# Performance work log

Measured on AMD Instinct MI355X. Metric: run time of the kernel, lower is better.

Reference implementation:

```python
import jax, jax.numpy as jnp
import numpy as np


def setup_inputs() -> dict:
    key = jax.random.key(0)
    ks = jax.random.split(key, 10)
    B, C, T, H, W = 1, 512, 8, 32, 32
    x = jax.random.normal(ks[0], (B, C, T, H, W), dtype=jnp.float32)
    gamma = jnp.ones((C,), dtype=jnp.float32)  # RMSNorm gamma (shape (C,1,1,1) in torch)
    std = 0.02
    wq = jax.random.normal(ks[1], (C, C), dtype=jnp.float32) * std
    bq = jnp.zeros((C,), dtype=jnp.float32)
    wk = jax.random.normal(ks[2], (C, C), dtype=jnp.float32) * std
    bk = jnp.zeros((C,), dtype=jnp.float32)
    wv = jax.random.normal(ks[3], (C, C), dtype=jnp.float32) * std
    bv = jnp.zeros((C,), dtype=jnp.float32)
    wo = jax.random.normal(ks[4], (C, C), dtype=jnp.float32) * std
    bo = jnp.zeros((C,), dtype=jnp.float32)
    return {"x": x, "gamma": gamma, "wq": wq, "bq": bq, "wk": wk, "bk": bk,
            "wv": wv, "bv": bv, "wo": wo, "bo": bo}


def _conv1(w, b, h):
    # 1x1x1 Conv3d == per-position channel matmul. h: [B,C,T,H,W]
    return jnp.einsum('oc,bcthw->bothw', w, h) + b[None, :, None, None, None]


def reference(x, gamma, wq, bq, wk, bk, wv, bv, wo, bo):
    B, C, T, H, W = x.shape
    n_hw = H * W
    S = T * n_hw
    scale = C ** 0.5

    # RMS norm over channel dim (F.normalize dim=1, eps=1e-12) * sqrt(C) * gamma
    norm = jnp.sqrt(jnp.sum(x * x, axis=1, keepdims=True))
    xn = x / jnp.maximum(norm, 1e-12) * scale * gamma[None, :, None, None, None]

    q = _conv1(wq, bq, xn).reshape(B, C, S).transpose(0, 2, 1)  # [B,S,C]
    k = _conv1(wk, bk, xn).reshape(B, C, S).transpose(0, 2, 1)
    v = _conv1(wv, bv, xn).reshape(B, C, S).transpose(0, 2, 1)

    # frame-block causal mask: token i (frame fi) attends to j with frame fj <= fi
    frame = jnp.arange(S) // n_hw
    allowed = frame[None, :] <= frame[:, None]  # [S,S] bool

    scores = jnp.einsum('bic,bjc->bij', q, k) / np.sqrt(C).astype(np.float32)
    scores = jnp.where(allowed[None], scores, -jnp.inf)
    attn = jax.nn.softmax(scores, axis=-1)
    o = jnp.einsum('bij,bjc->bic', attn, v)  # [B,S,C]

    o = o.transpose(0, 2, 1).reshape(B, C, T, H, W)
    out = _conv1(wo, bo, o) + x
    return out
```

## Files before the change

kernel.cpp:

```cpp
#include <hip/hip_runtime.h>
#include <stdint.h>


typedef __bf16 bf16;
typedef __bf16 bf16x8 __attribute__((ext_vector_type(8)));
typedef float f32x4 __attribute__((ext_vector_type(4)));
typedef uint32_t u32;
typedef uint32_t u32x2 __attribute__((ext_vector_type(2)));

#define MFMA16(a, b, c) __builtin_amdgcn_mfma_f32_16x16x32_bf16((a), (b), (c), 0, 0, 0)

__device__ __forceinline__ u32 pack2(float a, float b) {
  union { bf16 h[2]; u32 u; } x;
  x.h[0] = (bf16)a;
  x.h[1] = (bf16)b;
  return x.u;
}

__device__ __forceinline__ void async_copy16(const bf16* gsrc, bf16* ldst) {
  __builtin_amdgcn_global_load_lds(
      (const __attribute__((address_space(1))) void*)gsrc,
      (__attribute__((address_space(3))) void*)ldst, 16, 0, 0);
}

__global__ void cvt_w_kernel(const float* __restrict__ a, const float* __restrict__ b,
                             const float* __restrict__ c, const float* __restrict__ d,
                             bf16* __restrict__ out) {
  int i = blockIdx.x * 256 + threadIdx.x;
  const int N = 512 * 512;
  out[i]         = (bf16)a[i];
  out[N + i]     = (bf16)b[i];
  out[2 * N + i] = (bf16)c[i];
  out[3 * N + i] = (bf16)d[i];
}

__global__ __launch_bounds__(256) void rmsnorm_kernel(const float* __restrict__ x,
                                                      const float* __restrict__ gamma,
                                                      bf16* __restrict__ xn) {
  const int S = 8192;
  __shared__ float sums[4][64];
  int ts = threadIdx.x & 63, tc = threadIdx.x >> 6;
  int s = blockIdx.x * 64 + ts;
  float acc = 0.f;
  for (int c = tc * 128; c < tc * 128 + 128; ++c) {
    float v = x[(size_t)c * S + s];
    acc += v * v;
  }
  sums[tc][ts] = acc;
  __syncthreads();
  float tot = sums[0][ts] + sums[1][ts] + sums[2][ts] + sums[3][ts];
  float kk = 22.62741699796952f / fmaxf(sqrtf(tot), 1e-12f);
  for (int c0 = tc * 128; c0 < tc * 128 + 128; c0 += 8) {
    bf16x8 o;
#pragma unroll
    for (int j = 0; j < 8; ++j) o[j] = (bf16)(x[(size_t)(c0 + j) * S + s] * kk * gamma[c0 + j]);
    *(bf16x8*)(xn + (size_t)s * 512 + c0) = o;
  }
}

template <int EPI>
__global__ __launch_bounds__(256, 2) void gemm_nt_kernel(const bf16* __restrict__ A,
                                                         const bf16* __restrict__ B,
                                                         const float* __restrict__ bias0,
                                                         const float* __restrict__ bias1,
                                                         const float* __restrict__ resid,
                                                         void* __restrict__ Cout0,
                                                         void* __restrict__ Cout1, int M, int N,
                                                         int nbn) {
  __shared__ bf16 a_lds[2][128 * 64];
  __shared__ bf16 b_lds[2][128 * 64];
  const int K = 512;
  int bm = blockIdx.x / nbn, bn = blockIdx.x % nbn;
  int m0 = bm * 128, n0 = bn * 128;
  int tid = threadIdx.x, lane = tid & 63;
  int wid = tid >> 6;
  int wm = (wid >> 1) * 64, wn = (wid & 1) * 64;
  int l15 = lane & 15, l4 = lane >> 4;
  f32x4 acc[4][4];
#pragma unroll
  for (int i = 0; i < 4; ++i)
#pragma unroll
    for (int j = 0; j < 4; ++j) acc[i][j] = (f32x4){0.f, 0.f, 0.f, 0.f};

  auto stage = [&](int buf, int k0) {
#pragma unroll
    for (int j = 0; j < 4; ++j) {
      int r = wid * 32 + j * 8 + (lane >> 3);
      int cs = ((lane & 7) ^ (r & 7)) << 3;
      async_copy16(A + (size_t)(m0 + r) * K + k0 + cs, &a_lds[buf][(wid * 32 + j * 8) << 6]);
      async_copy16(B + (size_t)(n0 + r) * K + k0 + cs, &b_lds[buf][(wid * 32 + j * 8) << 6]);
    }
  };

  stage(0, 0);
  int buf = 0;
  int swk = l15 & 7;
  for (int t = 0; t < 8; ++t) {
    if (t < 7) {
      stage(buf ^ 1, (t + 1) * 64);
      asm volatile("s_waitcnt vmcnt(8)" ::: "memory");
    } else {
      asm volatile("s_waitcnt vmcnt(0)" ::: "memory");
    }
    __builtin_amdgcn_s_barrier();
#pragma unroll
    for (int kk = 0; kk < 2; ++kk) {
      bf16x8 af[4], bfr[4];
#pragma unroll
      for (int i = 0; i < 4; ++i)
        af[i] = *(bf16x8*)(&a_lds[buf][((wm + i * 16 + l15) << 6) + (((kk * 4 + l4) ^ swk) << 3)]);
#pragma unroll
      for (int j = 0; j < 4; ++j)
        bfr[j] = *(bf16x8*)(&b_lds[buf][((wn + j * 16 + l15) << 6) + (((kk * 4 + l4) ^ swk) << 3)]);
#pragma unroll
      for (int i = 0; i < 4; ++i)
#pragma unroll
        for (int j = 0; j < 4; ++j) acc[i][j] = MFMA16(af[i], bfr[j], acc[i][j]);
    }
    __builtin_amdgcn_s_barrier();
    buf ^= 1;
  }
#pragma unroll
  for (int i = 0; i < 4; ++i)
#pragma unroll
    for (int j = 0; j < 4; ++j) {
      int col = n0 + wn + j * 16 + l15;
#pragma unroll
      for (int r = 0; r < 4; ++r) {
        int row = m0 + wm + i * 16 + l4 * 4 + r;
        float v = acc[i][j][r];
        if (EPI == 0) {
          bf16* o = (bf16*)(col < 512 ? Cout0 : Cout1);
          const float* bb = col < 512 ? bias0 : bias1;
          int cc = col & 511;
          o[(size_t)row * 512 + cc] = (bf16)(v + bb[cc]);
        } else if (EPI == 1) {
          size_t idx = (size_t)row * N + col;
          ((float*)Cout0)[idx] = v + bias0[row] + resid[idx];
        } else {
          ((bf16*)Cout0)[(size_t)row * N + col] = (bf16)(v + bias0[row]);
        }
      }
    }
}

__global__ __launch_bounds__(256, 2) void attn_kernel(const bf16* __restrict__ Qg,
                                                      const bf16* __restrict__ Kg,
                                                      const bf16* __restrict__ VT,
                                                      bf16* __restrict__ Oat,
                                                      bf16* __restrict__ Opart,
                                                      float2* __restrict__ mlbuf) {
  const float SC2 = 1.4426950408889634f / 22.627416997969522f;
  __shared__ bf16 k_lds[32 * 512];
  __shared__ bf16 vt_lds[512 * 32];

  int b = (blockIdx.x & 7) * 64 + (blockIdx.x >> 3);
  int f = 0, cxe = 0, np = 1;
  while (b >= 16 * np) { b -= 16 * np; cxe += np - 1; ++f; np = (f < 4) ? f + 1 : f; }
  int p = b >> 4, qi = b & 15;
  int q0 = f * 1024 + qi * 64;
  int ntf = (f + 1) * 32;
  int t0 = (p * ntf) / np, t1 = ((p + 1) * ntf) / np;

  int tid = threadIdx.x, wid = tid >> 6, lane = tid & 63;
  int l15 = lane & 15, l4 = lane >> 4;

  int qrow = q0 + wid * 16 + l15;
  bf16x8 qreg[16];
#pragma unroll
  for (int ks = 0; ks < 16; ++ks)
    qreg[ks] = *(const bf16x8*)(Qg + (size_t)qrow * 512 + ks * 32 + l4 * 8);

  f32x4 oacc[32];
#pragma unroll
  for (int i = 0; i < 32; ++i) oacc[i] = (f32x4){0.f, 0.f, 0.f, 0.f};
  float lsum = 0.f;

  auto stageK = [&](int t) {
    int kv0 = t * 32;
#pragma unroll
    for (int i = 0; i < 8; ++i) {
      int rr = wid * 8 + i;
      int g = (rr & 3) | (((rr >> 3) & 1) << 2);
      async_copy16(Kg + (((size_t)(kv0 + rr)) << 9) + ((lane ^ g) << 3), &k_lds[rr << 9]);
    }
  };
  auto stageV = [&](int t) {
    int kv0 = t * 32;
#pragma unroll
    for (int i = 0; i < 8; ++i) {
      int rr = wid * 8 + i;
      async_copy16(VT + (size_t)(rr * 16 + (lane >> 2)) * 8192 + kv0 +
                       (((lane & 3) ^ ((lane >> 3) & 3)) << 3),
                   &vt_lds[rr << 9]);
    }
  };

  stageK(t0);
  stageV(t0);

  int gk = (l15 & 3) | (((l15 >> 2) & 1) << 2);
  int ra = ((l15 >> 2) * 8 + (l15 & 3)) << 9;
  int rb = ra + (4 << 9);
  int svw = (l15 >> 1) & 3;

  for (int t = t0; t < t1; ++t) {
    asm volatile("s_waitcnt vmcnt(8)" ::: "memory");
    __builtin_amdgcn_s_barrier();

    f32x4 sacca = {0.f, 0.f, 0.f, 0.f}, saccb = sacca;
    __builtin_amdgcn_s_setprio(1);
#pragma unroll
    for (int ks = 0; ks < 16; ++ks) {
      int c0 = ((ks * 4 + l4) ^ gk) << 3;
      bf16x8 a0 = *(const bf16x8*)(k_lds + ra + c0);
      bf16x8 a1 = *(const bf16x8*)(k_lds + rb + c0);
      sacca = MFMA16(a0, qreg[ks], sacca);
      saccb = MFMA16(a1, qreg[ks], saccb);
    }
    __builtin_amdgcn_s_setprio(0);

    float pra[4], prb[4];
    float ps = 0.f;
#pragma unroll
    for (int r = 0; r < 4; ++r) {
      pra[r] = exp2f(sacca[r] * SC2);
      prb[r] = exp2f(saccb[r] * SC2);
      ps += pra[r] + prb[r];
    }
    lsum += ps;

    union { u32 d[4]; bf16x8 v; } pf;
    pf.d[0] = pack2(pra[0], pra[1]);
    pf.d[1] = pack2(pra[2], pra[3]);
    pf.d[2] = pack2(prb[0], prb[1]);
    pf.d[3] = pack2(prb[2], prb[3]);

    asm volatile("s_waitcnt vmcnt(0)" ::: "memory");
    __builtin_amdgcn_s_barrier();

    if (t + 1 < t1) stageK(t + 1);

    __builtin_amdgcn_s_setprio(1);
#pragma unroll
    for (int df = 0; df < 32; ++df) {
      bf16x8 vf = *(const bf16x8*)(vt_lds + (df * 16 + l15) * 32 + ((l4 ^ svw) << 3));
      oacc[df] = MFMA16(vf, pf.v, oacc[df]);
    }
    __builtin_amdgcn_s_setprio(0);

    __builtin_amdgcn_s_barrier();
    if (t + 1 < t1) stageV(t + 1);
  }

  lsum += __shfl_xor(lsum, 16);
  lsum += __shfl_xor(lsum, 32);

  int qr = q0 + wid * 16 + l15;
  bf16* op = (p == 0) ? Oat + (size_t)qr * 512
                      : Opart + ((size_t)(cxe + p - 1) * 1024 + (qr & 1023)) * 512;
#pragma unroll
  for (int df = 0; df < 32; ++df) {
    u32x2 w2 = {pack2(oacc[df][0], oacc[df][1]), pack2(oacc[df][2], oacc[df][3])};
    *(u32x2*)(op + df * 16 + l4 * 4) = w2;
  }
  if (l4 == 0) mlbuf[p * 8192 + qr] = make_float2(0.f, lsum);
}

__global__ void combine_kernel(const bf16* __restrict__ Opart, const float2* __restrict__ ml,
                               bf16* __restrict__ O) {
  int i = blockIdx.x * 256 + threadIdx.x;
  int row = i >> 6, dc = (i & 63) * 8;
  int f = row >> 10;
  int np = f + (f < 4 ? 1 : 0);
  int cxe = f * (f - 1) / 2 - (f > 4 ? f - 4 : 0);
  float2 m0 = ml[row];
  float mm = m0.x;
  for (int p = 1; p < np; ++p) mm = fmaxf(mm, ml[p * 8192 + row].x);
  float acc[8];
  float denom;
  {
    float w = exp2f(m0.x - mm);
    denom = w * m0.y;
    bf16x8 o = *(const bf16x8*)(O + (size_t)row * 512 + dc);
#pragma unroll
    for (int j = 0; j < 8; ++j) acc[j] = w * (float)o[j];
  }
  int rowin = row & 1023;
  for (int p = 1; p < np; ++p) {
    float2 mp = ml[p * 8192 + row];
    float w = exp2f(mp.x - mm);
    denom += w * mp.y;
    bf16x8 o = *(const bf16x8*)(Opart + ((size_t)(cxe + p - 1) * 1024 + rowin) * 512 + dc);
#pragma unroll
    for (int j = 0; j < 8; ++j) acc[j] += w * (float)o[j];
  }
  float inv = 1.f / denom;
  bf16x8 r;
#pragma unroll
  for (int j = 0; j < 8; ++j) r[j] = (bf16)(acc[j] * inv);
  *(bf16x8*)(O + (size_t)row * 512 + dc) = r;
}

extern "C" void kernel_launch(void* const* d_in, const int* in_sizes, int n_in, void* d_out,
                              int out_size, void* d_ws, size_t ws_size, hipStream_t stream) {
  (void)in_sizes; (void)n_in; (void)out_size; (void)ws_size;
  const float* x = (const float*)d_in[0];
  const float* gamma = (const float*)d_in[1];
  const float* wq = (const float*)d_in[2];
  const float* bq = (const float*)d_in[3];
  const float* wk = (const float*)d_in[4];
  const float* bk = (const float*)d_in[5];
  const float* wv = (const float*)d_in[6];
  const float* bv = (const float*)d_in[7];
  const float* wo = (const float*)d_in[8];
  const float* bo = (const float*)d_in[9];

  const size_t SC = (size_t)8192 * 512;
  bf16* wq_b = (bf16*)d_ws;
  bf16* wk_b = wq_b + 262144;
  bf16* wv_b = wk_b + 262144;
  bf16* wo_b = wv_b + 262144;
  bf16* xn_oat = wo_b + 262144;
  bf16* q = xn_oat + SC;
  bf16* k = q + SC;
  bf16* vt = k + SC;
  bf16* opart = vt + SC;
  float2* ml = (float2*)(opart + (size_t)24 * 1024 * 512);

  cvt_w_kernel<<<1024, 256, 0, stream>>>(wq, wk, wv, wo, wq_b);
  rmsnorm_kernel<<<128, 256, 0, stream>>>(x, gamma, xn_oat);
  gemm_nt_kernel<0><<<512, 256, 0, stream>>>(xn_oat, wq_b, bq, bk, nullptr, q, k, 8192, 1024, 8);
  gemm_nt_kernel<2><<<256, 256, 0, stream>>>(wv_b, xn_oat, bv, nullptr, nullptr, vt, nullptr, 512,
                                             8192, 64);
  attn_kernel<<<512, 256, 0, stream>>>(q, k, vt, xn_oat, opart, ml);
  combine_kernel<<<2048, 256, 0, stream>>>(opart, ml, xn_oat);
  gemm_nt_kernel<1><<<256, 256, 0, stream>>>(wo_b, xn_oat, bo, nullptr, x, d_out, nullptr, 512,
                                             8192, 64);
}
```

Baseline: 212.8 us.

## Share P tiles via LDS so each wave computes a D-slice for all query rows

Each wave writes its bf16 probability fragment to LDS, then reads all four waves' fragments and computes the PV product for a 128-wide slice of the head dimension across all 64 query rows. Before, each wave read the full 512-wide V^T tile from LDS for its own 16 rows. Now each V fragment is loaded once and reused across four MFMAs, cutting LDS read traffic for V by about four times. The cost is an extra LDS write and read of P plus an lgkmcnt wait before the barrier. The output store layout is reorganised to match.

Result: slower. 268.9 us (+26.3%).

```diff
diff --git a/kernel.cpp b/kernel.cpp
--- a/kernel.cpp
+++ b/kernel.cpp
@@ -153,6 +153,7 @@
   const float SC2 = 1.4426950408889634f / 22.627416997969522f;
   __shared__ bf16 k_lds[32 * 512];
   __shared__ bf16 vt_lds[512 * 32];
+  __shared__ bf16 p_lds[4][16 * 40];
 
   int b = (blockIdx.x & 7) * 64 + (blockIdx.x >> 3);
   int f = 0, cxe = 0, np = 1;
@@ -235,17 +236,23 @@
     pf.d[1] = pack2(pra[2], pra[3]);
     pf.d[2] = pack2(prb[0], prb[1]);
     pf.d[3] = pack2(prb[2], prb[3]);
-
-    asm volatile("s_waitcnt vmcnt(0)" ::: "memory");
+    *(bf16x8*)(&p_lds[wid][l15 * 40 + l4 * 8]) = pf.v;
+
+    asm volatile("s_waitcnt vmcnt(0) lgkmcnt(0)" ::: "memory");
     __builtin_amdgcn_s_barrier();
 
     if (t + 1 < t1) stageK(t + 1);
 
+    bf16x8 pfr[4];
+#pragma unroll
+    for (int s = 0; s < 4; ++s) pfr[s] = *(const bf16x8*)(&p_lds[s][l15 * 40 + l4 * 8]);
     __builtin_amdgcn_s_setprio(1);
 #pragma unroll
-    for (int df = 0; df < 32; ++df) {
-      bf16x8 vf = *(const bf16x8*)(vt_lds + (df * 16 + l15) * 32 + ((l4 ^ svw) << 3));
-      oacc[df] = MFMA16(vf, pf.v, oacc[df]);
+    for (int dt = 0; dt < 8; ++dt) {
+      bf16x8 vf =
+          *(const bf16x8*)(vt_lds + (wid * 128 + dt * 16 + l15) * 32 + ((l4 ^ svw) << 3));
+#pragma unroll
+      for (int s = 0; s < 4; ++s) oacc[dt * 4 + s] = MFMA16(vf, pfr[s], oacc[dt * 4 + s]);
     }
     __builtin_amdgcn_s_setprio(0);
 
@@ -256,15 +263,19 @@
   lsum += __shfl_xor(lsum, 16);
   lsum += __shfl_xor(lsum, 32);
 
-  int qr = q0 + wid * 16 + l15;
-  bf16* op = (p == 0) ? Oat + (size_t)qr * 512
-                      : Opart + ((size_t)(cxe + p - 1) * 1024 + (qr & 1023)) * 512;
-#pragma unroll
-  for (int df = 0; df < 32; ++df) {
-    u32x2 w2 = {pack2(oacc[df][0], oacc[df][1]), pack2(oacc[df][2], oacc[df][3])};
-    *(u32x2*)(op + df * 16 + l4 * 4) = w2;
-  }
-  if (l4 == 0) mlbuf[p * 8192 + qr] = make_float2(0.f, lsum);
+  bf16* obase = (p == 0) ? Oat : Opart + ((size_t)(cxe + p - 1) * 1024) * 512;
+#pragma unroll
+  for (int s = 0; s < 4; ++s) {
+    int qr = q0 + s * 16 + l15;
+    int qloc = (p == 0) ? qr : (qr & 1023);
+    bf16* op = obase + (size_t)qloc * 512 + wid * 128 + l4 * 4;
+#pragma unroll
+    for (int dt = 0; dt < 8; ++dt) {
+      f32x4 o = oacc[dt * 4 + s];
+      *(u32x2*)(op + dt * 16) = (u32x2){pack2(o[0], o[1]), pack2(o[2], o[3])};
+    }
+  }
+  if (l4 == 0) mlbuf[p * 8192 + q0 + wid * 16 + l15] = make_float2(0.f, lsum);
 }
 
 __global__ void combine_kernel(const bf16* __restrict__ Opart, const float2* __restrict__ ml,
```

## Merge prep and projection launches, defer softmax normalization into output GEMM

Applied to the files above, without the earlier changes.

Weight conversion and RMSNorm now run in one launch, split by block index. The Q/K and V projection GEMMs are likewise merged into a single launch. The combine kernel drops the max-based rescaling, because the stored max is always zero. It now only sums partial outputs for rows that have several partials, and writes a per-row inverse denominator. The output GEMM applies that inverse per token column in its epilogue. This removes two kernel launches and some elementwise work in combine, at the cost of a bf16 intermediate that is no longer normalized and some branching in the merged kernels.

Result: slower. 220.0 us (+3.4%).

```diff
diff --git a/kernel.cpp b/kernel.cpp
--- a/kernel.cpp
+++ b/kernel.cpp
@@ -23,22 +23,25 @@
       (__attribute__((address_space(3))) void*)ldst, 16, 0, 0);
 }
 
-__global__ void cvt_w_kernel(const float* __restrict__ a, const float* __restrict__ b,
-                             const float* __restrict__ c, const float* __restrict__ d,
-                             bf16* __restrict__ out) {
-  int i = blockIdx.x * 256 + threadIdx.x;
-  const int N = 512 * 512;
-  out[i]         = (bf16)a[i];
-  out[N + i]     = (bf16)b[i];
-  out[2 * N + i] = (bf16)c[i];
-  out[3 * N + i] = (bf16)d[i];
-}
-
-__global__ __launch_bounds__(256) void rmsnorm_kernel(const float* __restrict__ x,
-                                                      const float* __restrict__ gamma,
-                                                      bf16* __restrict__ xn) {
+__global__ __launch_bounds__(256) void prep_kernel(const float* __restrict__ x,
+                                                   const float* __restrict__ gamma,
+                                                   bf16* __restrict__ xn,
+                                                   const float* __restrict__ wq,
+                                                   const float* __restrict__ wk,
+                                                   const float* __restrict__ wv,
+                                                   const float* __restrict__ wo,
+                                                   bf16* __restrict__ wout) {
+  __shared__ float sums[4][64];
+  if (blockIdx.x >= 128) {
+    int i = (blockIdx.x - 128) * 256 + threadIdx.x;
+    const int N = 512 * 512;
+    wout[i]         = (bf16)wq[i];
+    wout[N + i]     = (bf16)wk[i];
+    wout[2 * N + i] = (bf16)wv[i];
+    wout[3 * N + i] = (bf16)wo[i];
+    return;
+  }
   const int S = 8192;
-  __shared__ float sums[4][64];
   int ts = threadIdx.x & 63, tc = threadIdx.x >> 6;
   int s = blockIdx.x * 64 + ts;
   float acc = 0.f;
@@ -58,19 +61,28 @@
   }
 }
 
-template <int EPI>
-__global__ __launch_bounds__(256, 2) void gemm_nt_kernel(const bf16* __restrict__ A,
-                                                         const bf16* __restrict__ B,
-                                                         const float* __restrict__ bias0,
-                                                         const float* __restrict__ bias1,
-                                                         const float* __restrict__ resid,
-                                                         void* __restrict__ Cout0,
-                                                         void* __restrict__ Cout1, int M, int N,
-                                                         int nbn) {
+__global__ __launch_bounds__(256, 2) void proj_kernel(const bf16* __restrict__ xn,
+                                                      const bf16* __restrict__ wqk,
+                                                      const float* __restrict__ bq,
+                                                      const float* __restrict__ bk,
+                                                      bf16* __restrict__ qo,
+                                                      bf16* __restrict__ ko,
+                                                      const bf16* __restrict__ wv,
+                                                      const float* __restrict__ bv,
+                                                      bf16* __restrict__ vt) {
   __shared__ bf16 a_lds[2][128 * 64];
   __shared__ bf16 b_lds[2][128 * 64];
   const int K = 512;
-  int bm = blockIdx.x / nbn, bn = blockIdx.x % nbn;
+  bool qkmode = blockIdx.x < 512;
+  const bf16* A;
+  const bf16* B;
+  int bidx, nbn, N;
+  if (qkmode) {
+    A = xn; B = wqk; bidx = blockIdx.x; nbn = 8; N = 1024;
+  } else {
+    A = wv; B = xn; bidx = blockIdx.x - 512; nbn = 64; N = 8192;
+  }
+  int bm = bidx / nbn, bn = bidx % nbn;
   int m0 = bm * 128, n0 = bn * 128;
   int tid = threadIdx.x, lane = tid & 63;
   int wid = tid >> 6;
@@ -129,17 +141,89 @@
       for (int r = 0; r < 4; ++r) {
         int row = m0 + wm + i * 16 + l4 * 4 + r;
         float v = acc[i][j][r];
-        if (EPI == 0) {
-          bf16* o = (bf16*)(col < 512 ? Cout0 : Cout1);
-          const float* bb = col < 512 ? bias0 : bias1;
+        if (qkmode) {
+          bf16* o = col < 512 ? qo : ko;
+          const float* bb = col < 512 ? bq : bk;
           int cc = col & 511;
           o[(size_t)row * 512 + cc] = (bf16)(v + bb[cc]);
-        } else if (EPI == 1) {
-          size_t idx = (size_t)row * N + col;
-          ((float*)Cout0)[idx] = v + bias0[row] + resid[idx];
         } else {
-          ((bf16*)Cout0)[(size_t)row * N + col] = (bf16)(v + bias0[row]);
+          vt[(size_t)row * N + col] = (bf16)(v + bv[row]);
         }
+      }
+    }
+}
+
+__global__ __launch_bounds__(256, 2) void gemm_out_kernel(const bf16* __restrict__ A,
+                                                          const bf16* __restrict__ B,
+                                                          const float* __restrict__ bias,
+                                                          const float* __restrict__ inv,
+                                                          const float* __restrict__ resid,
+                                                          float* __restrict__ Cout) {
+  __shared__ bf16 a_lds[2][128 * 64];
+  __shared__ bf16 b_lds[2][128 * 64];
+  const int K = 512;
+  const int N = 8192;
+  int bm = blockIdx.x / 64, bn = blockIdx.x % 64;
+  int m0 = bm * 128, n0 = bn * 128;
+  int tid = threadIdx.x, lane = tid & 63;
+  int wid = tid >> 6;
+  int wm = (wid >> 1) * 64, wn = (wid & 1) * 64;
+  int l15 = lane & 15, l4 = lane >> 4;
+  f32x4 acc[4][4];
+#pragma unroll
+  for (int i = 0; i < 4; ++i)
+#pragma unroll
+    for (int j = 0; j < 4; ++j) acc[i][j] = (f32x4){0.f, 0.f, 0.f, 0.f};
+
+  auto stage = [&](int buf, int k0) {
+#pragma unroll
+    for (int j = 0; j < 4; ++j) {
+      int r = wid * 32 + j * 8 + (lane >> 3);
+      int cs = ((lane & 7) ^ (r & 7)) << 3;
+      async_copy16(A + (size_t)(m0 + r) * K + k0 + cs, &a_lds[buf][(wid * 32 + j * 8) << 6]);
+      async_copy16(B + (size_t)(n0 + r) * K + k0 + cs, &b_lds[buf][(wid * 32 + j * 8) << 6]);
+    }
+  };
+
+  stage(0, 0);
+  int buf = 0;
+  int swk = l15 & 7;
+  for (int t = 0; t < 8; ++t) {
+    if (t < 7) {
+      stage(buf ^ 1, (t + 1) * 64);
+      asm volatile("s_waitcnt vmcnt(8)" ::: "memory");
+    } else {
+      asm volatile("s_waitcnt vmcnt(0)" ::: "memory");
+    }
+    __builtin_amdgcn_s_barrier();
+#pragma unroll
+    for (int kk = 0; kk < 2; ++kk) {
+      bf16x8 af[4], bfr[4];
+#pragma unroll
+      for (int i = 0; i < 4; ++i)
+        af[i] = *(bf16x8*)(&a_lds[buf][((wm + i * 16 + l15) << 6) + (((kk * 4 + l4) ^ swk) << 3)]);
+#pragma unroll
+      for (int j = 0; j < 4; ++j)
+        bfr[j] = *(bf16x8*)(&b_lds[buf][((wn + j * 16 + l15) << 6) + (((kk * 4 + l4) ^ swk) << 3)]);
+#pragma unroll
+      for (int i = 0; i < 4; ++i)
+#pragma unroll
+        for (int j = 0; j < 4; ++j) acc[i][j] = MFMA16(af[i], bfr[j], acc[i][j]);
+    }
+    __builtin_amdgcn_s_barrier();
+    buf ^= 1;
+  }
+#pragma unroll
+  for (int i = 0; i < 4; ++i)
+#pragma unroll
+    for (int j = 0; j < 4; ++j) {
+      int col = n0 + wn + j * 16 + l15;
+      float iv = inv[col];
+#pragma unroll
+      for (int r = 0; r < 4; ++r) {
+        int row = m0 + wm + i * 16 + l4 * 4 + r;
+        size_t idx = (size_t)row * N + col;
+        Cout[idx] = acc[i][j][r] * iv + bias[row] + resid[idx];
       }
     }
 }
@@ -268,38 +352,33 @@
 }
 
 __global__ void combine_kernel(const bf16* __restrict__ Opart, const float2* __restrict__ ml,
-                               bf16* __restrict__ O) {
+                               bf16* __restrict__ O, float* __restrict__ invd) {
   int i = blockIdx.x * 256 + threadIdx.x;
   int row = i >> 6, dc = (i & 63) * 8;
   int f = row >> 10;
   int np = f + (f < 4 ? 1 : 0);
   int cxe = f * (f - 1) / 2 - (f > 4 ? f - 4 : 0);
-  float2 m0 = ml[row];
-  float mm = m0.x;
-  for (int p = 1; p < np; ++p) mm = fmaxf(mm, ml[p * 8192 + row].x);
-  float acc[8];
-  float denom;
-  {
-    float w = exp2f(m0.x - mm);
-    denom = w * m0.y;
+  if ((i & 63) == 0) {
+    float den = ml[row].y;
+    for (int p = 1; p < np; ++p) den += ml[p * 8192 + row].y;
+    invd[row] = 1.f / den;
+  }
+  if (np > 1) {
+    float acc[8];
     bf16x8 o = *(const bf16x8*)(O + (size_t)row * 512 + dc);
 #pragma unroll
-    for (int j = 0; j < 8; ++j) acc[j] = w * (float)o[j];
-  }
-  int rowin = row & 1023;
-  for (int p = 1; p < np; ++p) {
-    float2 mp = ml[p * 8192 + row];
-    float w = exp2f(mp.x - mm);
-    denom += w * mp.y;
-    bf16x8 o = *(const bf16x8*)(Opart + ((size_t)(cxe + p - 1) * 1024 + rowin) * 512 + dc);
-#pragma unroll
-    for (int j = 0; j < 8; ++j) acc[j] += w * (float)o[j];
-  }
-  float inv = 1.f / denom;
-  bf16x8 r;
-#pragma unroll
-  for (int j = 0; j < 8; ++j) r[j] = (bf16)(acc[j] * inv);
-  *(bf16x8*)(O + (size_t)row * 512 + dc) = r;
+    for (int j = 0; j < 8; ++j) acc[j] = (float)o[j];
+    int rowin = row & 1023;
+    for (int p = 1; p < np; ++p) {
+      bf16x8 op = *(const bf16x8*)(Opart + ((size_t)(cxe + p - 1) * 1024 + rowin) * 512 + dc);
+#pragma unroll
+      for (int j = 0; j < 8; ++j) acc[j] += (float)op[j];
+    }
+    bf16x8 r;
+#pragma unroll
+    for (int j = 0; j < 8; ++j) r[j] = (bf16)acc[j];
+    *(bf16x8*)(O + (size_t)row * 512 + dc) = r;
+  }
 }
 
 extern "C" void kernel_launch(void* const* d_in, const int* in_sizes, int n_in, void* d_out,
@@ -327,14 +406,12 @@
   bf16* vt = k + SC;
   bf16* opart = vt + SC;
   float2* ml = (float2*)(opart + (size_t)24 * 1024 * 512);
-
-  cvt_w_kernel<<<1024, 256, 0, stream>>>(wq, wk, wv, wo, wq_b);
-  rmsnorm_kernel<<<128, 256, 0, stream>>>(x, gamma, xn_oat);
-  gemm_nt_kernel<0><<<512, 256, 0, stream>>>(xn_oat, wq_b, bq, bk, nullptr, q, k, 8192, 1024, 8);
-  gemm_nt_kernel<2><<<256, 256, 0, stream>>>(wv_b, xn_oat, bv, nullptr, nullptr, vt, nullptr, 512,
-                                             8192, 64);
+  float* invd = (float*)(ml + 7 * 8192);
+
+  (void)wk; (void)wv; (void)wo;
+  prep_kernel<<<1152, 256, 0, stream>>>(x, gamma, xn_oat, wq, wk, wv, wo, wq_b);
+  proj_kernel<<<768, 256, 0, stream>>>(xn_oat, wq_b, bq, bk, q, k, wv_b, bv, vt);
   attn_kernel<<<512, 256, 0, stream>>>(q, k, vt, xn_oat, opart, ml);
-  combine_kernel<<<2048, 256, 0, stream>>>(opart, ml, xn_oat);
-  gemm_nt_kernel<1><<<256, 256, 0, stream>>>(wo_b, xn_oat, bo, nullptr, x, d_out, nullptr, 512,
-                                             8192, 64);
-}
+  combine_kernel<<<2048, 256, 0, stream>>>(opart, ml, xn_oat, invd);
+  gemm_out_kernel<<<256, 256, 0, stream>>>(wo_b, xn_oat, bo, invd, x, (float*)d_out);
+}
```
